# Kernel tuning notes

Measured on AMD Instinct MI355X. Metric: run time of the kernel, lower is better.

The kernel has to match this reference:

```python
import jax, jax.numpy as jnp
import numpy as np

B, N, S, D = 32, 2048, 64, 1024  # batch, num_options (bank size), num_selected, feature dim


def setup_inputs() -> dict:
    key = jax.random.key(0)
    k1, k2, k3, k4 = jax.random.split(key, 4)
    state = jax.random.normal(k1, (B, N, D), dtype=jnp.float32)
    substate = jax.random.normal(k2, (B, S, D), dtype=jnp.float32)
    selection_index = jax.random.randint(k3, (B, S), 0, N, dtype=jnp.int64)
    selection_probabilities = jax.random.uniform(k4, (B, S), dtype=jnp.float32)
    return {
        "state": state,
        "substate": substate,
        "selection_index": selection_index,
        "selection_probabilities": selection_probabilities,
    }


def reference(state, substate, selection_index, selection_probabilities):
    # virtual_state_scatter with dim=1, superposition=False.
    # Gather the currently-stored virtual layers at the selected indices,
    # interpolate toward the new substate values by the selection probabilities,
    # and scatter the interpolated rows back into state.
    idx = selection_index  # (B, S) int
    p = selection_probabilities[:, :, None]  # (B, S, 1) broadcast over features
    gathered = jnp.take_along_axis(state, idx[:, :, None], axis=1)  # (B, S, D)
    interpolated = (1.0 - p) * gathered + p * substate  # (B, S, D)
    # matching torch.scatter's unspecified-duplicate semantics).
    updated = jax.vmap(lambda s, i, v: s.at[i].set(v))(state, idx, interpolated)
    return updated
```

## Files before the change

### kernel.cpp

```cpp
#include <hip/hip_runtime.h>

constexpr int B = 32;
constexpr int N = 2048;
constexpr int S = 64;
constexpr int D = 1024;
constexpr int ROW4 = D / 4;
constexpr long TOTAL4 = (long)B * N * ROW4;
constexpr int GRID  = 2048;
constexpr int BLOCK = 256;
constexpr int ITERS = (int)(TOTAL4 / ((long)GRID * BLOCK));

typedef float f4 __attribute__((ext_vector_type(4)));

__global__ void setup_winner(const int* __restrict__ idx,
                             int* __restrict__ winner) {
    for (int i = threadIdx.x; i < B * N; i += blockDim.x) winner[i] = -1;
    __syncthreads();
    for (int t = threadIdx.x; t < B * S; t += blockDim.x) {
        int b = t >> 6;
        int s = t & (S - 1);
        atomicMax(&winner[b * N + idx[t]], s);
    }
}

__global__ __launch_bounds__(BLOCK) void fused_update(
    const f4* __restrict__ state, const f4* __restrict__ substate,
    const float* __restrict__ probs, const int* __restrict__ winner,
    f4* __restrict__ out) {
    const long stride = (long)GRID * BLOCK;
    const long base = (long)blockIdx.x * BLOCK + threadIdx.x;
#pragma unroll 4
    for (int it = 0; it < ITERS; ++it) {
        long gid = base + (long)it * stride;
        int row = (int)(gid >> 8);
        int e   = (int)(gid & (ROW4 - 1));
        int w = winner[row];
        f4 g = __builtin_nontemporal_load(&state[gid]);
        f4 o;
        if (w >= 0) {
            int b  = row >> 11;
            int bs = b * S + w;
            float p = probs[bs];
            f4 v = substate[(long)bs * ROW4 + e];
            o = (1.0f - p) * g + p * v;
        } else {
            o = g;
        }
        __builtin_nontemporal_store(o, &out[gid]);
    }
}

extern "C" void kernel_launch(void* const* d_in, const int* in_sizes, int n_in,
                              void* d_out, int out_size, void* d_ws, size_t ws_size,
                              hipStream_t stream) {
    const f4*    state    = (const f4*)d_in[0];
    const f4*    substate = (const f4*)d_in[1];
    const int*   idx      = (const int*)d_in[2];
    const float* probs    = (const float*)d_in[3];
    f4*          out      = (f4*)d_out;
    int*         winner   = (int*)d_ws;

    setup_winner<<<1, 1024, 0, stream>>>(idx, winner);
    fused_update<<<GRID, BLOCK, 0, stream>>>(state, substate, probs, winner, out);
}
```

Before: 109.4 us.

## Fuse winner-table setup into update kernel using per-block shared memory

Drops the separate single-block setup kernel that filled a global winner table for the last-write-wins resolution. Each block now builds the winner table for its own batch in shared memory with shared atomics, then streams one contiguous chunk of that batch's rows. This removes a serial kernel launch and its global-memory dependency. The cost is that every block redundantly initialises an 8 KB shared table and runs two barriers, and the grid changes from a grid-stride layout to per-batch chunks.

```diff
diff --git a/kernel.cpp b/kernel.cpp
--- a/kernel.cpp
+++ b/kernel.cpp
@@ -5,46 +5,45 @@
 constexpr int S = 64;
 constexpr int D = 1024;
 constexpr int ROW4 = D / 4;
-constexpr long TOTAL4 = (long)B * N * ROW4;
-constexpr int GRID  = 2048;
 constexpr int BLOCK = 256;
-constexpr int ITERS = (int)(TOTAL4 / ((long)GRID * BLOCK));
+constexpr int CHUNKS_PER_BATCH = 64;
+constexpr int ROWS_PER_CHUNK = N / CHUNKS_PER_BATCH;
+constexpr int F4_PER_CHUNK = ROWS_PER_CHUNK * ROW4;
+constexpr int ITERS = F4_PER_CHUNK / BLOCK;
+constexpr int GRID = B * CHUNKS_PER_BATCH;
 
 typedef float f4 __attribute__((ext_vector_type(4)));
 
-__global__ void setup_winner(const int* __restrict__ idx,
-                             int* __restrict__ winner) {
-    for (int i = threadIdx.x; i < B * N; i += blockDim.x) winner[i] = -1;
-    __syncthreads();
-    for (int t = threadIdx.x; t < B * S; t += blockDim.x) {
-        int b = t >> 6;
-        int s = t & (S - 1);
-        atomicMax(&winner[b * N + idx[t]], s);
-    }
-}
-
 __global__ __launch_bounds__(BLOCK) void fused_update(
     const f4* __restrict__ state, const f4* __restrict__ substate,
-    const float* __restrict__ probs, const int* __restrict__ winner,
+    const float* __restrict__ probs, const int* __restrict__ idx,
     f4* __restrict__ out) {
-    const long stride = (long)GRID * BLOCK;
-    const long base = (long)blockIdx.x * BLOCK + threadIdx.x;
+    __shared__ int win[N];
+    const int b = blockIdx.x >> 6;
+    const int chunk = blockIdx.x & 63;
+
+    for (int i = threadIdx.x; i < N; i += BLOCK) win[i] = 0;
+    __syncthreads();
+    if (threadIdx.x < S)
+        atomicMax(&win[idx[b * S + threadIdx.x]], threadIdx.x + 1);
+    __syncthreads();
+
+    const long batchBase = (long)b * (N * ROW4);
+    const int chunkBase = chunk * F4_PER_CHUNK;
 #pragma unroll 4
     for (int it = 0; it < ITERS; ++it) {
-        long gid = base + (long)it * stride;
-        int row = (int)(gid >> 8);
-        int e   = (int)(gid & (ROW4 - 1));
-        int w = winner[row];
+        int off = chunkBase + it * BLOCK + threadIdx.x;
+        long gid = batchBase + off;
+        int row = off >> 8;
+        int e   = off & (ROW4 - 1);
+        int w = win[row];
         f4 g = __builtin_nontemporal_load(&state[gid]);
-        f4 o;
-        if (w >= 0) {
-            int b  = row >> 11;
-            int bs = b * S + w;
+        f4 o = g;
+        if (w > 0) {
+            int bs = (b << 6) + (w - 1);
             float p = probs[bs];
             f4 v = substate[(long)bs * ROW4 + e];
             o = (1.0f - p) * g + p * v;
-        } else {
-            o = g;
         }
         __builtin_nontemporal_store(o, &out[gid]);
     }
@@ -58,8 +57,6 @@
     const int*   idx      = (const int*)d_in[2];
     const float* probs    = (const float*)d_in[3];
     f4*          out      = (f4*)d_out;
-    int*         winner   = (int*)d_ws;
 
-    setup_winner<<<1, 1024, 0, stream>>>(idx, winner);
-    fused_update<<<GRID, BLOCK, 0, stream>>>(state, substate, probs, winner, out);
+    fused_update<<<GRID, BLOCK, 0, stream>>>(state, substate, probs, idx, out);
 }
```

Result: faster. 106.7 us (-2.4%).

## Split update into bulk copy plus per-selected-row fixup kernel

Applied to the files above, without the earlier changes.

Replaces the winner-table setup kernel and the fused per-element update with two kernels. The first is a plain streaming copy of state to out, and the second is a small per-(batch, selection) kernel that computes the interpolated row and writes it. Duplicate indices are resolved by having each selection skip itself if a later selection targets the same row. This removes the serial single-block setup kernel and the per-element winner lookups and branches. In exchange it rereads the selected rows after the copy and drops the nontemporal load/store hints.

```diff
diff --git a/kernel.cpp b/kernel.cpp
--- a/kernel.cpp
+++ b/kernel.cpp
@@ -6,48 +6,42 @@
 constexpr int D = 1024;
 constexpr int ROW4 = D / 4;
 constexpr long TOTAL4 = (long)B * N * ROW4;
+constexpr int BLOCK = 256;
 constexpr int GRID  = 2048;
-constexpr int BLOCK = 256;
 constexpr int ITERS = (int)(TOTAL4 / ((long)GRID * BLOCK));
 
 typedef float f4 __attribute__((ext_vector_type(4)));
 
-__global__ void setup_winner(const int* __restrict__ idx,
-                             int* __restrict__ winner) {
-    for (int i = threadIdx.x; i < B * N; i += blockDim.x) winner[i] = -1;
-    __syncthreads();
-    for (int t = threadIdx.x; t < B * S; t += blockDim.x) {
-        int b = t >> 6;
-        int s = t & (S - 1);
-        atomicMax(&winner[b * N + idx[t]], s);
+__global__ __launch_bounds__(BLOCK) void pure_copy(const f4* __restrict__ src,
+                                                   f4* __restrict__ dst) {
+    const long stride = (long)GRID * BLOCK;
+    long gid = (long)blockIdx.x * BLOCK + threadIdx.x;
+#pragma unroll 8
+    for (int it = 0; it < ITERS; ++it, gid += stride) {
+        dst[gid] = src[gid];
     }
 }
 
-__global__ __launch_bounds__(BLOCK) void fused_update(
-    const f4* __restrict__ state, const f4* __restrict__ substate,
-    const float* __restrict__ probs, const int* __restrict__ winner,
-    f4* __restrict__ out) {
-    const long stride = (long)GRID * BLOCK;
-    const long base = (long)blockIdx.x * BLOCK + threadIdx.x;
-#pragma unroll 4
-    for (int it = 0; it < ITERS; ++it) {
-        long gid = base + (long)it * stride;
-        int row = (int)(gid >> 8);
-        int e   = (int)(gid & (ROW4 - 1));
-        int w = winner[row];
-        f4 g = __builtin_nontemporal_load(&state[gid]);
-        f4 o;
-        if (w >= 0) {
-            int b  = row >> 11;
-            int bs = b * S + w;
-            float p = probs[bs];
-            f4 v = substate[(long)bs * ROW4 + e];
-            o = (1.0f - p) * g + p * v;
-        } else {
-            o = g;
-        }
-        __builtin_nontemporal_store(o, &out[gid]);
-    }
+__global__ __launch_bounds__(BLOCK) void fixup(const f4* __restrict__ state,
+                                               const f4* __restrict__ substate,
+                                               const float* __restrict__ probs,
+                                               const int* __restrict__ idx,
+                                               f4* __restrict__ out) {
+    const int b = blockIdx.x >> 6;
+    const int s = blockIdx.x & (S - 1);
+    __shared__ int sidx[S];
+    if (threadIdx.x < S) sidx[threadIdx.x] = idx[b * S + threadIdx.x];
+    __syncthreads();
+    const int n = sidx[s];
+    for (int t = s + 1; t < S; ++t)
+        if (sidx[t] == n) return;
+    const float p = probs[b * S + s];
+    const long rowBase = ((long)b * N + n) * ROW4;
+    const long subBase = ((long)b * S + s) * ROW4;
+    const int e = threadIdx.x;
+    f4 g = state[rowBase + e];
+    f4 v = substate[subBase + e];
+    out[rowBase + e] = (1.0f - p) * g + p * v;
 }
 
 extern "C" void kernel_launch(void* const* d_in, const int* in_sizes, int n_in,
@@ -58,8 +52,7 @@
     const int*   idx      = (const int*)d_in[2];
     const float* probs    = (const float*)d_in[3];
     f4*          out      = (f4*)d_out;
-    int*         winner   = (int*)d_ws;
 
-    setup_winner<<<1, 1024, 0, stream>>>(idx, winner);
-    fused_update<<<GRID, BLOCK, 0, stream>>>(state, substate, probs, winner, out);
+    pure_copy<<<GRID, BLOCK, 0, stream>>>(state, out);
+    fixup<<<B * S, BLOCK, 0, stream>>>(state, substate, probs, idx, out);
 }
```

Result: slower. 156.8 us (+43.3%).
